# Optimization experiments

Hardware: AMD Instinct MI355X
Metric: run time of the kernel (lower is better)

The kernel has to match this reference:

```python
import jax, jax.numpy as jnp
import numpy as np

B, C = 16, 256          # batch, feature_dim
P, K = 20, 50           # max_polygons, max_points
H4 = W4 = 32            # p4 spatial
H2 = W2 = 128           # p2 spatial


def setup_inputs() -> dict:
    key = jax.random.key(0)
    ks = jax.random.split(key, 12)

    def w(k, shape, fan_in):
        return jax.random.normal(k, shape, jnp.float32) * (1.0 / np.sqrt(fan_in))

    return {
        "p4": jax.random.normal(ks[0], (B, C, H4, W4), jnp.float32),
        "p2": jax.random.normal(ks[1], (B, C, H2, W2), jnp.float32),
        "segmentation": jax.random.uniform(ks[2], (B, 1, H2, W2), dtype=jnp.float32),
        # init_net linears (torch layout: [out, in])
        "W1": w(ks[3], (1024, C * 64), C * 64), "b1": jnp.zeros((1024,), jnp.float32),
        "W2": w(ks[4], (P * K * 2, 1024), 1024), "b2": jnp.zeros((P * K * 2,), jnp.float32),
        # refine_net
        "R1": w(ks[5], (128, C + 2), C + 2), "rb1": jnp.zeros((128,), jnp.float32),
        "R2": w(ks[6], (64, 128), 128), "rb2": jnp.zeros((64,), jnp.float32),
        "R3": w(ks[7], (2, 64), 64), "rb3": jnp.zeros((2,), jnp.float32),
        # validity_net
        "V1": w(ks[8], (128, K * 2), K * 2), "vb1": jnp.zeros((128,), jnp.float32),
        "V2": w(ks[9], (1, 128), 128), "vb2": jnp.zeros((1,), jnp.float32),
    }


def _bilinear_sample(img, xy):
    """F.grid_sample(align_corners=False, padding='zeros') for one image.
    img: [C, H, W]; xy: [N, 2] in [-1, 1] with xy[:, 0]=x (width), xy[:, 1]=y (height).
    Returns [N, C]."""
    Cc, H, W = img.shape
    x = ((xy[:, 0] + 1.0) * W - 1.0) * 0.5
    y = ((xy[:, 1] + 1.0) * H - 1.0) * 0.5
    x0 = jnp.floor(x)
    y0 = jnp.floor(y)
    wx1 = x - x0
    wy1 = y - y0

    def corner(xi, yi, wgt):
        valid = (xi >= 0) & (xi <= W - 1) & (yi >= 0) & (yi <= H - 1)
        xc = jnp.clip(xi, 0, W - 1).astype(jnp.int32)
        yc = jnp.clip(yi, 0, H - 1).astype(jnp.int32)
        v = img[:, yc, xc]  # [C, N]
        return v * (wgt * valid.astype(img.dtype))[None, :]

    out = (corner(x0, y0, (1 - wx1) * (1 - wy1))
           + corner(x0 + 1, y0, wx1 * (1 - wy1))
           + corner(x0, y0 + 1, (1 - wx1) * wy1)
           + corner(x0 + 1, y0 + 1, wx1 * wy1))
    return out.T  # [N, C]


def reference(p4, p2, segmentation, W1, b1, W2, b2, R1, rb1, R2, rb2, R3, rb3, V1, vb1, V2, vb2):
    Bn, Cc, h4, w4 = p4.shape
    pooled = p4.reshape(Bn, Cc, 8, h4 // 8, 8, w4 // 8).mean(axis=(3, 5))
    flat = pooled.reshape(Bn, -1)                       # [B, C*64]
    h = jax.nn.relu(flat @ W1.T + b1)
    init_pts = jax.nn.sigmoid(h @ W2.T + b2).reshape(Bn, P, K, 2)

    # refine: grid_sample point gather + 3-layer MLP
    grid = init_pts * 2.0 - 1.0                          # [B, P, K, 2]
    xy = grid.reshape(Bn, -1, 2)                         # [B, N=P*K, 2]
    sampled = jax.vmap(_bilinear_sample)(p2, xy)         # [B, N, C]
    coords = init_pts.reshape(Bn, -1, 2)
    feat = jnp.concatenate([sampled, coords], axis=-1)   # [B, N, C+2]
    h1 = jax.nn.relu(feat @ R1.T + rb1)
    h2 = jax.nn.relu(h1 @ R2.T + rb2)
    disp = jnp.tanh(h2 @ R3.T + rb3).reshape(Bn, P, K, 2)
    refined = jnp.clip(init_pts + 0.1 * disp, 0.0, 1.0)

    # validity
    pf = refined.reshape(Bn * P, K * 2)
    v = jax.nn.sigmoid(jax.nn.relu(pf @ V1.T + vb1) @ V2.T + vb2).reshape(Bn, P)
    return refined, v, init_pts
```

## Files before the change

### kernel.cpp

```cpp
#include <hip/hip_runtime.h>
#include <hip/hip_bf16.h>
#include <math.h>

#define NB 16
#define NC 256
#define NPTS 1000
#define NN2 2000
#define D1 1024
#define KFLAT 16384

__global__ __launch_bounds__(256) void k_pool(const float* __restrict__ p4,
                                              float* __restrict__ flat) {
    int o = blockIdx.x * 256 + threadIdx.x;
    int bc = o >> 6;
    int ij = o & 63;
    int i = ij >> 3, j = ij & 7;
    const float* src = p4 + ((size_t)bc * 32 + i * 4) * 32 + j * 4;
    float s = 0.f;
#pragma unroll
    for (int di = 0; di < 4; ++di) {
        float4 v = *reinterpret_cast<const float4*>(src + di * 32);
        s += v.x + v.y + v.z + v.w;
    }
    flat[o] = s * (1.0f / 16.0f);
}

__global__ __launch_bounds__(256) void k_fc1(const float* __restrict__ flat,
                                             const float* __restrict__ W1,
                                             const float* __restrict__ b1,
                                             float* __restrict__ h) {
    __shared__ float lds[16 * 256];
    const int tid = threadIdx.x;
    const int wave = tid >> 6, lane = tid & 63;
    const int n = blockIdx.x * 4 + wave;
    float acc[16];
#pragma unroll
    for (int m = 0; m < 16; ++m) acc[m] = 0.f;
    const float4* W1r  = reinterpret_cast<const float4*>(W1 + (size_t)n * KFLAT);
    const float4* flat4 = reinterpret_cast<const float4*>(flat);
    float4* lds4 = reinterpret_cast<float4*>(lds);
    for (int kt = 0; kt < KFLAT; kt += 256) {
        __syncthreads();
#pragma unroll
        for (int r = 0; r < 4; ++r) {
            int idx4 = tid + r * 256;
            int m = idx4 >> 6, off = idx4 & 63;
            lds4[m * 64 + off] = flat4[m * (KFLAT / 4) + (kt >> 2) + off];
        }
        __syncthreads();
        float4 w = W1r[(kt >> 2) + lane];
#pragma unroll
        for (int m = 0; m < 16; ++m) {
            float4 f = lds4[m * 64 + lane];
            acc[m] += w.x * f.x + w.y * f.y + w.z * f.z + w.w * f.w;
        }
    }
#pragma unroll
    for (int m = 0; m < 16; ++m) {
        float v = acc[m];
#pragma unroll
        for (int off = 32; off > 0; off >>= 1) v += __shfl_xor(v, off, 64);
        acc[m] = v;
    }
    if (lane == 0) {
        float bias = b1[n];
#pragma unroll
        for (int m = 0; m < 16; ++m)
            h[m * D1 + n] = fmaxf(acc[m] + bias, 0.f);
    }
}

__global__ __launch_bounds__(256) void k_fc2(const float* __restrict__ h,
                                             const float* __restrict__ W2,
                                             const float* __restrict__ b2,
                                             float* __restrict__ init_ws,
                                             float* __restrict__ out_init) {
    const int tid = threadIdx.x;
    const int wave = tid >> 6, lane = tid & 63;
    const int n = blockIdx.x * 4 + wave;
    float acc[16];
#pragma unroll
    for (int m = 0; m < 16; ++m) acc[m] = 0.f;
    const float4* W2r = reinterpret_cast<const float4*>(W2 + (size_t)n * D1);
    const float4* h4  = reinterpret_cast<const float4*>(h);
#pragma unroll
    for (int it = 0; it < 4; ++it) {
        int k4 = it * 64 + lane;
        float4 w = W2r[k4];
#pragma unroll
        for (int m = 0; m < 16; ++m) {
            float4 f = h4[m * 256 + k4];
            acc[m] += w.x * f.x + w.y * f.y + w.z * f.z + w.w * f.w;
        }
    }
    float bias = b2[n];
#pragma unroll
    for (int m = 0; m < 16; ++m) {
        float v = acc[m];
#pragma unroll
        for (int off = 32; off > 0; off >>= 1) v += __shfl_xor(v, off, 64);
        if (lane == 0) {
            float s = 1.f / (1.f + expf(-(v + bias)));
            init_ws[m * NN2 + n] = s;
            out_init[m * NN2 + n] = s;
        }
    }
}

__global__ __launch_bounds__(256) void k_sample(const float* __restrict__ p2,
                                                const float* __restrict__ init_ws,
                                                __hip_bfloat16* __restrict__ sampled) {
    const int bc = blockIdx.x;
    const int b = bc >> 8;
    const float* img = p2 + (size_t)bc * (128 * 128);
    const float* ip = init_ws + b * NN2;
    for (int n = threadIdx.x; n < NPTS; n += 256) {
        float sx = ip[2 * n], sy = ip[2 * n + 1];
        float x = sx * 128.f - 0.5f;
        float y = sy * 128.f - 0.5f;
        float x0f = floorf(x), y0f = floorf(y);
        float wx = x - x0f, wy = y - y0f;
        int x0 = (int)x0f, y0 = (int)y0f;
        int x1 = x0 + 1, y1 = y0 + 1;
        bool vx0 = (x0 >= 0) && (x0 <= 127);
        bool vx1 = (x1 >= 0) && (x1 <= 127);
        bool vy0 = (y0 >= 0) && (y0 <= 127);
        bool vy1 = (y1 >= 0) && (y1 <= 127);
        int cx0 = min(max(x0, 0), 127), cx1 = min(max(x1, 0), 127);
        int cy0 = min(max(y0, 0), 127), cy1 = min(max(y1, 0), 127);
        float v00 = (vx0 && vy0) ? img[cy0 * 128 + cx0] : 0.f;
        float v10 = (vx1 && vy0) ? img[cy0 * 128 + cx1] : 0.f;
        float v01 = (vx0 && vy1) ? img[cy1 * 128 + cx0] : 0.f;
        float v11 = (vx1 && vy1) ? img[cy1 * 128 + cx1] : 0.f;
        float r = v00 * (1.f - wx) * (1.f - wy) + v10 * wx * (1.f - wy)
                + v01 * (1.f - wx) * wy + v11 * wx * wy;
        sampled[(size_t)bc * NPTS + n] = __float2bfloat16(r);
    }
}

__global__ __launch_bounds__(256) void k_r1(const __hip_bfloat16* __restrict__ sampled,
                                            const float* __restrict__ init_ws,
                                            const float* __restrict__ R1,
                                            const float* __restrict__ rb1,
                                            float* __restrict__ h1) {
    __shared__ float As[64][128];
    __shared__ float Bs[64][64];
    const int tid = threadIdx.x;
    const int b = blockIdx.x >> 4;
    const int n0 = (blockIdx.x & 15) * 64;
    const int jt = tid & 15;
    const int nt = tid >> 4;
    float acc[8][4];
#pragma unroll
    for (int a = 0; a < 8; ++a)
#pragma unroll
        for (int m = 0; m < 4; ++m) acc[a][m] = 0.f;

    for (int k0 = 0; k0 < 256; k0 += 64) {
        __syncthreads();
        for (int idx = tid; idx < 128 * 64; idx += 256) {
            int kk = idx >> 7, r = idx & 127;
            As[kk][r] = R1[r * 258 + k0 + kk];
        }
        for (int idx = tid; idx < 64 * 64; idx += 256) {
            int r = idx >> 6, col = idx & 63;
            int n = n0 + col;
            Bs[r][col] = (n < NPTS)
                ? __bfloat162float(sampled[((size_t)(b * 256 + k0 + r)) * NPTS + n])
                : 0.f;
        }
        __syncthreads();
#pragma unroll 8
        for (int kk = 0; kk < 64; ++kk) {
            float4 a0 = *reinterpret_cast<const float4*>(&As[kk][jt * 4]);
            float4 a1 = *reinterpret_cast<const float4*>(&As[kk][64 + jt * 4]);
            float4 bb = *reinterpret_cast<const float4*>(&Bs[kk][nt * 4]);
            float av[8] = {a0.x, a0.y, a0.z, a0.w, a1.x, a1.y, a1.z, a1.w};
            float bv[4] = {bb.x, bb.y, bb.z, bb.w};
#pragma unroll
            for (int a = 0; a < 8; ++a)
#pragma unroll
                for (int m = 0; m < 4; ++m) acc[a][m] += av[a] * bv[m];
        }
    }
    float xs[4] = {0, 0, 0, 0}, ys[4] = {0, 0, 0, 0};
    int ns[4];
#pragma unroll
    for (int m = 0; m < 4; ++m) {
        int n = n0 + nt * 4 + m;
        ns[m] = n;
        if (n < NPTS) {
            xs[m] = init_ws[b * NN2 + 2 * n];
            ys[m] = init_ws[b * NN2 + 2 * n + 1];
        }
    }
#pragma unroll
    for (int a = 0; a < 8; ++a) {
        int j = (a < 4) ? (jt * 4 + a) : (64 + jt * 4 + (a - 4));
        float rx = R1[j * 258 + 256];
        float ry = R1[j * 258 + 257];
        float bj = rb1[j];
#pragma unroll
        for (int m = 0; m < 4; ++m) {
            int n = ns[m];
            if (n < NPTS) {
                float v = acc[a][m] + rx * xs[m] + ry * ys[m] + bj;
                h1[((size_t)(b * NPTS + n)) * 128 + j] = fmaxf(v, 0.f);
            }
        }
    }
}

__global__ __launch_bounds__(256) void k_r23(const float* __restrict__ h1,
                                             const float* __restrict__ init_ws,
                                             const float* __restrict__ R2,
                                             const float* __restrict__ rb2,
                                             const float* __restrict__ R3,
                                             const float* __restrict__ rb3,
                                             float* __restrict__ refined) {
    __shared__ float R2t[128][64];
    __shared__ float r3[2][64];
    __shared__ float rb2s[64];
    __shared__ float hbuf[4][128];
    const int tid = threadIdx.x, wave = tid >> 6, lane = tid & 63;
    for (int idx = tid; idx < 64 * 128; idx += 256) {
        int j = idx & 63, k = idx >> 6;
        R2t[k][j] = R2[j * 128 + k];
    }
    if (tid < 128) r3[tid >> 6][tid & 63] = R3[tid];
    if (tid < 64) rb2s[tid] = rb2[tid];
    __syncthreads();
    const float b30 = rb3[0], b31 = rb3[1];
    const int wgid = blockIdx.x * 4 + wave;
    for (int it = 0; it < 16; ++it) {
        int pt = wgid + it * 1000;
        __syncthreads();
        hbuf[wave][lane] = h1[(size_t)pt * 128 + lane];
        hbuf[wave][64 + lane] = h1[(size_t)pt * 128 + 64 + lane];
        __syncthreads();
        float a = rb2s[lane];
#pragma unroll 16
        for (int k = 0; k < 128; ++k)
            a += R2t[k][lane] * hbuf[wave][k];
        a = fmaxf(a, 0.f);
        float d0 = r3[0][lane] * a;
        float d1 = r3[1][lane] * a;
#pragma unroll
        for (int off = 32; off > 0; off >>= 1) {
            d0 += __shfl_xor(d0, off, 64);
            d1 += __shfl_xor(d1, off, 64);
        }
        if (lane == 0) {
            float ix = init_ws[it * NN2 + 2 * wgid];
            float iy = init_ws[it * NN2 + 2 * wgid + 1];
            float rx = ix + 0.1f * tanhf(d0 + b30);
            float ry = iy + 0.1f * tanhf(d1 + b31);
            refined[(size_t)pt * 2]     = fminf(fmaxf(rx, 0.f), 1.f);
            refined[(size_t)pt * 2 + 1] = fminf(fmaxf(ry, 0.f), 1.f);
        }
    }
}

__global__ __launch_bounds__(256) void k_vhead(const float* __restrict__ refined,
                                               const float* __restrict__ V1,
                                               const float* __restrict__ vb1,
                                               const float* __restrict__ V2,
                                               const float* __restrict__ vb2,
                                               float* __restrict__ vout) {
    __shared__ float V1t[100][128];
    __shared__ float pf[4][100];
    const int tid = threadIdx.x, wave = tid >> 6, lane = tid & 63;
    for (int idx = tid; idx < 100 * 128; idx += 256) {
        int j = idx & 127, k = idx >> 7;
        V1t[k][j] = V1[j * 100 + k];
    }
    __syncthreads();
    const int row = blockIdx.x * 4 + wave;
    const float* src = refined + row * 100;
    if (lane < 50) {
        pf[wave][lane] = src[lane];
        pf[wave][lane + 50] = src[lane + 50];
    }
    __syncthreads();
    float a0 = vb1[lane], a1 = vb1[64 + lane];
#pragma unroll 10
    for (int k = 0; k < 100; ++k) {
        float p = pf[wave][k];
        a0 += V1t[k][lane] * p;
        a1 += V1t[k][64 + lane] * p;
    }
    float s = fmaxf(a0, 0.f) * V2[lane] + fmaxf(a1, 0.f) * V2[64 + lane];
#pragma unroll
    for (int off = 32; off > 0; off >>= 1) s += __shfl_xor(s, off, 64);
    if (lane == 0) vout[row] = 1.f / (1.f + expf(-(s + vb2[0])));
}

extern "C" void kernel_launch(void* const* d_in, const int* in_sizes, int n_in,
                              void* d_out, int out_size, void* d_ws, size_t ws_size,
                              hipStream_t stream) {
    const float* p4  = (const float*)d_in[0];
    const float* p2  = (const float*)d_in[1];
    const float* W1  = (const float*)d_in[3];
    const float* b1  = (const float*)d_in[4];
    const float* W2  = (const float*)d_in[5];
    const float* b2  = (const float*)d_in[6];
    const float* R1  = (const float*)d_in[7];
    const float* rb1 = (const float*)d_in[8];
    const float* R2  = (const float*)d_in[9];
    const float* rb2 = (const float*)d_in[10];
    const float* R3  = (const float*)d_in[11];
    const float* rb3 = (const float*)d_in[12];
    const float* V1  = (const float*)d_in[13];
    const float* vb1 = (const float*)d_in[14];
    const float* V2  = (const float*)d_in[15];
    const float* vb2 = (const float*)d_in[16];
    float* out = (float*)d_out;

    char* ws = (char*)d_ws;
    float* flat = (float*)(ws + 0);
    float* h    = (float*)(ws + 1048576);
    float* ipts = (float*)(ws + 1114112);
    float* h1   = (float*)(ws + 1242112);
    __hip_bfloat16* samp = (__hip_bfloat16*)(ws + 9434112);

    k_pool<<<1024, 256, 0, stream>>>(p4, flat);
    k_fc1<<<256, 256, 0, stream>>>(flat, W1, b1, h);
    k_fc2<<<500, 256, 0, stream>>>(h, W2, b2, ipts, out + 32320);
    k_sample<<<4096, 256, 0, stream>>>(p2, ipts, samp);
    k_r1<<<256, 256, 0, stream>>>(samp, ipts, R1, rb1, h1);
    k_r23<<<250, 256, 0, stream>>>(h1, ipts, R2, rb2, R3, rb3, out);
    k_vhead<<<80, 256, 0, stream>>>(out, V1, vb1, V2, vb2, out + 32000);
}
```

Before: 556.3 us.

## Pretranspose weights, split-K fc1, stage images in LDS, retile refine kernels

```diff
diff --git a/kernel.cpp b/kernel.cpp
--- a/kernel.cpp
+++ b/kernel.cpp
@@ -8,6 +8,27 @@
 #define NN2 2000
 #define D1 1024
 #define KFLAT 16384
+
+__global__ __launch_bounds__(256) void k_prep(const float* __restrict__ R1,
+                                              const float* __restrict__ R2,
+                                              const float* __restrict__ V1,
+                                              float* __restrict__ R1t,
+                                              float* __restrict__ R2t_g,
+                                              float* __restrict__ V1t_g) {
+    int idx = blockIdx.x * 256 + threadIdx.x;
+    if (idx < 33024) {
+        int j = idx / 258, k = idx % 258;
+        R1t[k * 128 + j] = R1[idx];
+    } else if (idx < 33024 + 8192) {
+        int t = idx - 33024;
+        int j = t >> 7, k = t & 127;
+        R2t_g[k * 64 + j] = R2[t];
+    } else if (idx < 33024 + 8192 + 12800) {
+        int t = idx - 41216;
+        int j = t / 100, k = t % 100;
+        V1t_g[k * 128 + j] = V1[t];
+    }
+}
 
 __global__ __launch_bounds__(256) void k_pool(const float* __restrict__ p4,
                                               float* __restrict__ flat) {
@@ -25,33 +46,36 @@
     flat[o] = s * (1.0f / 16.0f);
 }
 
-__global__ __launch_bounds__(256) void k_fc1(const float* __restrict__ flat,
+__global__ __launch_bounds__(512) void k_fc1(const float* __restrict__ flat,
                                              const float* __restrict__ W1,
                                              const float* __restrict__ b1,
                                              float* __restrict__ h) {
-    __shared__ float lds[16 * 256];
+    __shared__ float lds[2 * 16 * 256];
     const int tid = threadIdx.x;
     const int wave = tid >> 6, lane = tid & 63;
-    const int n = blockIdx.x * 4 + wave;
+    const int colw = wave & 3, half = wave >> 2;
+    const int n = blockIdx.x * 4 + colw;
     float acc[16];
 #pragma unroll
     for (int m = 0; m < 16; ++m) acc[m] = 0.f;
-    const float4* W1r  = reinterpret_cast<const float4*>(W1 + (size_t)n * KFLAT);
+    const float4* W1r  = reinterpret_cast<const float4*>(W1 + (size_t)n * KFLAT + half * 8192);
     const float4* flat4 = reinterpret_cast<const float4*>(flat);
     float4* lds4 = reinterpret_cast<float4*>(lds);
-    for (int kt = 0; kt < KFLAT; kt += 256) {
+    for (int kt = 0; kt < 8192; kt += 256) {
         __syncthreads();
 #pragma unroll
         for (int r = 0; r < 4; ++r) {
-            int idx4 = tid + r * 256;
-            int m = idx4 >> 6, off = idx4 & 63;
-            lds4[m * 64 + off] = flat4[m * (KFLAT / 4) + (kt >> 2) + off];
+            int idx4 = tid + r * 512;
+            int hh = idx4 >> 10;
+            int m  = (idx4 >> 6) & 15;
+            int off = idx4 & 63;
+            lds4[idx4] = flat4[m * 4096 + hh * 2048 + (kt >> 2) + off];
         }
         __syncthreads();
         float4 w = W1r[(kt >> 2) + lane];
 #pragma unroll
         for (int m = 0; m < 16; ++m) {
-            float4 f = lds4[m * 64 + lane];
+            float4 f = lds4[half * 1024 + m * 64 + lane];
             acc[m] += w.x * f.x + w.y * f.y + w.z * f.z + w.w * f.w;
         }
     }
@@ -62,11 +86,16 @@
         for (int off = 32; off > 0; off >>= 1) v += __shfl_xor(v, off, 64);
         acc[m] = v;
     }
+    __syncthreads();
     if (lane == 0) {
-        float bias = b1[n];
-#pragma unroll
-        for (int m = 0; m < 16; ++m)
-            h[m * D1 + n] = fmaxf(acc[m] + bias, 0.f);
+#pragma unroll
+        for (int m = 0; m < 16; ++m) lds[wave * 16 + m] = acc[m];
+    }
+    __syncthreads();
+    if (tid < 64) {
+        int c = tid >> 4, m = tid & 15;
+        float v = lds[c * 16 + m] + lds[(c + 4) * 16 + m] + b1[blockIdx.x * 4 + c];
+        h[m * D1 + blockIdx.x * 4 + c] = fmaxf(v, 0.f);
     }
 }
 
@@ -110,9 +139,15 @@
 __global__ __launch_bounds__(256) void k_sample(const float* __restrict__ p2,
                                                 const float* __restrict__ init_ws,
                                                 __hip_bfloat16* __restrict__ sampled) {
+    __shared__ float img[128 * 128];
     const int bc = blockIdx.x;
     const int b = bc >> 8;
-    const float* img = p2 + (size_t)bc * (128 * 128);
+    const float4* src4 = reinterpret_cast<const float4*>(p2 + (size_t)bc * 16384);
+    float4* dst4 = reinterpret_cast<float4*>(img);
+#pragma unroll
+    for (int i = 0; i < 16; ++i)
+        dst4[threadIdx.x + i * 256] = src4[threadIdx.x + i * 256];
+    __syncthreads();
     const float* ip = init_ws + b * NN2;
     for (int n = threadIdx.x; n < NPTS; n += 256) {
         float sx = ip[2 * n], sy = ip[2 * n + 1];
@@ -140,30 +175,28 @@
 
 __global__ __launch_bounds__(256) void k_r1(const __hip_bfloat16* __restrict__ sampled,
                                             const float* __restrict__ init_ws,
-                                            const float* __restrict__ R1,
+                                            const float* __restrict__ R1t,
                                             const float* __restrict__ rb1,
                                             float* __restrict__ h1) {
     __shared__ float As[64][128];
-    __shared__ float Bs[64][64];
+    __shared__ float Bs[64][32];
     const int tid = threadIdx.x;
-    const int b = blockIdx.x >> 4;
-    const int n0 = (blockIdx.x & 15) * 64;
+    const int b = blockIdx.x >> 5;
+    const int n0 = (blockIdx.x & 31) * 32;
     const int jt = tid & 15;
     const int nt = tid >> 4;
-    float acc[8][4];
-#pragma unroll
-    for (int a = 0; a < 8; ++a)
-#pragma unroll
-        for (int m = 0; m < 4; ++m) acc[a][m] = 0.f;
+    float acc[8][2];
+#pragma unroll
+    for (int a = 0; a < 8; ++a) { acc[a][0] = 0.f; acc[a][1] = 0.f; }
 
     for (int k0 = 0; k0 < 256; k0 += 64) {
         __syncthreads();
         for (int idx = tid; idx < 128 * 64; idx += 256) {
             int kk = idx >> 7, r = idx & 127;
-            As[kk][r] = R1[r * 258 + k0 + kk];
-        }
-        for (int idx = tid; idx < 64 * 64; idx += 256) {
-            int r = idx >> 6, col = idx & 63;
+            As[kk][r] = R1t[(k0 + kk) * 128 + r];
+        }
+        for (int idx = tid; idx < 64 * 32; idx += 256) {
+            int r = idx >> 5, col = idx & 31;
             int n = n0 + col;
             Bs[r][col] = (n < NPTS)
                 ? __bfloat162float(sampled[((size_t)(b * 256 + k0 + r)) * NPTS + n])
@@ -174,20 +207,21 @@
         for (int kk = 0; kk < 64; ++kk) {
             float4 a0 = *reinterpret_cast<const float4*>(&As[kk][jt * 4]);
             float4 a1 = *reinterpret_cast<const float4*>(&As[kk][64 + jt * 4]);
-            float4 bb = *reinterpret_cast<const float4*>(&Bs[kk][nt * 4]);
+            float2 bb = *reinterpret_cast<const float2*>(&Bs[kk][nt * 2]);
             float av[8] = {a0.x, a0.y, a0.z, a0.w, a1.x, a1.y, a1.z, a1.w};
-            float bv[4] = {bb.x, bb.y, bb.z, bb.w};
-#pragma unroll
-            for (int a = 0; a < 8; ++a)
-#pragma unroll
-                for (int m = 0; m < 4; ++m) acc[a][m] += av[a] * bv[m];
-        }
-    }
-    float xs[4] = {0, 0, 0, 0}, ys[4] = {0, 0, 0, 0};
-    int ns[4];
-#pragma unroll
-    for (int m = 0; m < 4; ++m) {
-        int n = n0 + nt * 4 + m;
+            float bv[2] = {bb.x, bb.y};
+#pragma unroll
+            for (int a = 0; a < 8; ++a) {
+                acc[a][0] += av[a] * bv[0];
+                acc[a][1] += av[a] * bv[1];
+            }
+        }
+    }
+    float xs[2] = {0, 0}, ys[2] = {0, 0};
+    int ns[2];
+#pragma unroll
+    for (int m = 0; m < 2; ++m) {
+        int n = n0 + nt * 2 + m;
         ns[m] = n;
         if (n < NPTS) {
             xs[m] = init_ws[b * NN2 + 2 * n];
@@ -197,11 +231,11 @@
 #pragma unroll
     for (int a = 0; a < 8; ++a) {
         int j = (a < 4) ? (jt * 4 + a) : (64 + jt * 4 + (a - 4));
-        float rx = R1[j * 258 + 256];
-        float ry = R1[j * 258 + 257];
+        float rx = R1t[256 * 128 + j];
+        float ry = R1t[257 * 128 + j];
         float bj = rb1[j];
 #pragma unroll
-        for (int m = 0; m < 4; ++m) {
+        for (int m = 0; m < 2; ++m) {
             int n = ns[m];
             if (n < NPTS) {
                 float v = acc[a][m] + rx * xs[m] + ry * ys[m] + bj;
@@ -213,30 +247,42 @@
 
 __global__ __launch_bounds__(256) void k_r23(const float* __restrict__ h1,
                                              const float* __restrict__ init_ws,
-                                             const float* __restrict__ R2,
+                                             const float* __restrict__ R2t_g,
                                              const float* __restrict__ rb2,
                                              const float* __restrict__ R3,
                                              const float* __restrict__ rb3,
                                              float* __restrict__ refined) {
+    const int tid = threadIdx.x, wave = tid >> 6, lane = tid & 63;
+    const int wgid = blockIdx.x * 4 + wave;
+    const int n = wgid & 1023;
+    const int bbase = (wgid >> 10) * 8;
+    if (n >= 1000) return;
+
     __shared__ float R2t[128][64];
     __shared__ float r3[2][64];
     __shared__ float rb2s[64];
     __shared__ float hbuf[4][128];
-    const int tid = threadIdx.x, wave = tid >> 6, lane = tid & 63;
-    for (int idx = tid; idx < 64 * 128; idx += 256) {
-        int j = idx & 63, k = idx >> 6;
-        R2t[k][j] = R2[j * 128 + k];
-    }
+    for (int idx = tid; idx < 128 * 64; idx += 256)
+        R2t[idx >> 6][idx & 63] = R2t_g[idx];
     if (tid < 128) r3[tid >> 6][tid & 63] = R3[tid];
     if (tid < 64) rb2s[tid] = rb2[tid];
+
+    float hA[8], hB[8];
+#pragma unroll
+    for (int it = 0; it < 8; ++it) {
+        size_t pt = (size_t)(bbase + it) * 1000 + n;
+        hA[it] = h1[pt * 128 + lane];
+        hB[it] = h1[pt * 128 + 64 + lane];
+    }
     __syncthreads();
     const float b30 = rb3[0], b31 = rb3[1];
-    const int wgid = blockIdx.x * 4 + wave;
-    for (int it = 0; it < 16; ++it) {
-        int pt = wgid + it * 1000;
-        __syncthreads();
-        hbuf[wave][lane] = h1[(size_t)pt * 128 + lane];
-        hbuf[wave][64 + lane] = h1[(size_t)pt * 128 + 64 + lane];
+#pragma unroll
+    for (int it = 0; it < 8; ++it) {
+        int bb = bbase + it;
+        size_t pt = (size_t)bb * 1000 + n;
+        __syncthreads();
+        hbuf[wave][lane] = hA[it];
+        hbuf[wave][64 + lane] = hB[it];
         __syncthreads();
         float a = rb2s[lane];
 #pragma unroll 16
@@ -251,18 +297,18 @@
             d1 += __shfl_xor(d1, off, 64);
         }
         if (lane == 0) {
-            float ix = init_ws[it * NN2 + 2 * wgid];
-            float iy = init_ws[it * NN2 + 2 * wgid + 1];
+            float ix = init_ws[bb * NN2 + 2 * n];
+            float iy = init_ws[bb * NN2 + 2 * n + 1];
             float rx = ix + 0.1f * tanhf(d0 + b30);
             float ry = iy + 0.1f * tanhf(d1 + b31);
-            refined[(size_t)pt * 2]     = fminf(fmaxf(rx, 0.f), 1.f);
-            refined[(size_t)pt * 2 + 1] = fminf(fmaxf(ry, 0.f), 1.f);
+            refined[pt * 2]     = fminf(fmaxf(rx, 0.f), 1.f);
+            refined[pt * 2 + 1] = fminf(fmaxf(ry, 0.f), 1.f);
         }
     }
 }
 
 __global__ __launch_bounds__(256) void k_vhead(const float* __restrict__ refined,
-                                               const float* __restrict__ V1,
+                                               const float* __restrict__ V1t_g,
                                                const float* __restrict__ vb1,
                                                const float* __restrict__ V2,
                                                const float* __restrict__ vb2,
@@ -270,10 +316,8 @@
     __shared__ float V1t[100][128];
     __shared__ float pf[4][100];
     const int tid = threadIdx.x, wave = tid >> 6, lane = tid & 63;
-    for (int idx = tid; idx < 100 * 128; idx += 256) {
-        int j = idx & 127, k = idx >> 7;
-        V1t[k][j] = V1[j * 100 + k];
-    }
+    for (int idx = tid; idx < 100 * 128; idx += 256)
+        V1t[idx >> 7][idx & 127] = V1t_g[idx];
     __syncthreads();
     const int row = blockIdx.x * 4 + wave;
     const float* src = refined + row * 100;
@@ -322,12 +366,16 @@
     float* ipts = (float*)(ws + 1114112);
     float* h1   = (float*)(ws + 1242112);
     __hip_bfloat16* samp = (__hip_bfloat16*)(ws + 9434112);
-
+    float* R1t  = (float*)(ws + 17626112);
+    float* R2t_g= (float*)(ws + 17758208);
+    float* V1t_g= (float*)(ws + 17790976);
+
+    k_prep<<<212, 256, 0, stream>>>(R1, R2, V1, R1t, R2t_g, V1t_g);
     k_pool<<<1024, 256, 0, stream>>>(p4, flat);
-    k_fc1<<<256, 256, 0, stream>>>(flat, W1, b1, h);
+    k_fc1<<<256, 512, 0, stream>>>(flat, W1, b1, h);
     k_fc2<<<500, 256, 0, stream>>>(h, W2, b2, ipts, out + 32320);
     k_sample<<<4096, 256, 0, stream>>>(p2, ipts, samp);
-    k_r1<<<256, 256, 0, stream>>>(samp, ipts, R1, rb1, h1);
-    k_r23<<<250, 256, 0, stream>>>(h1, ipts, R2, rb2, R3, rb3, out);
-    k_vhead<<<80, 256, 0, stream>>>(out, V1, vb1, V2, vb2, out + 32000);
-}
+    k_r1<<<512, 256, 0, stream>>>(samp, ipts, R1t, rb1, h1);
+    k_r23<<<512, 256, 0, stream>>>(h1, ipts, R2t_g, rb2, R3, rb3, out);
+    k_vhead<<<80, 256, 0, stream>>>(out, V1t_g, vb1, V2, vb2, out + 32000);
+}
```

After: 584.3 us. 5.0% more time.
